# Kernel optimization log

Measured on AMD Instinct MI355X. Metric: run time of the kernel, lower is better.

## Reference

```python
import jax, jax.numpy as jnp
import numpy as np

D = 128      # d_model
H = 8        # n_heads
HD = D // H  # head_dim = 16
E = 256      # n_experts
R = 32       # kv_lora_rank
B, T = 4, 512
EPS = 1e-6


def _dense_init(k, fi, fo):
    s = float(1.0 / np.sqrt(fi))
    return jax.random.uniform(k, (fi, fo), minval=-s, maxval=s, dtype=jnp.float32)


def setup_inputs() -> dict:
    key = jax.random.key(0)
    ks = jax.random.split(key, 16)
    rng = np.random.RandomState(42)
    Q, _ = np.linalg.qr(rng.randn(D, D))
    glim = float(np.sqrt(6.0 / (D + D)))
    return {
        'x': jax.random.normal(ks[0], (B, T, D), dtype=jnp.float32),
        'g1': jnp.ones((D,), jnp.float32),
        'qW': _dense_init(ks[1], D, D), 'qb': jnp.zeros((D,), jnp.float32),
        'kdW': _dense_init(ks[2], D, R), 'kdb': jnp.zeros((R,), jnp.float32),
        'kuW': _dense_init(ks[3], R, 2 * D), 'kub': jnp.zeros((2 * D,), jnp.float32),
        'oW': _dense_init(ks[4], D, D), 'ob': jnp.zeros((D,), jnp.float32),
        'rot': jnp.asarray(Q, jnp.float32),
        'tq_scale': jnp.ones((D,), jnp.float32),
        's1W': _dense_init(ks[5], D, D), 's1b': jnp.zeros((D,), jnp.float32),
        's2W': _dense_init(ks[6], D, D), 's2b': jnp.zeros((D,), jnp.float32),
        'g2': jnp.ones((D,), jnp.float32),
        'gateW': _dense_init(ks[7], D, E), 'gateb': jnp.zeros((E,), jnp.float32),
        'expW': jax.random.uniform(ks[8], (E, D, D), minval=-glim, maxval=glim, dtype=jnp.float32),
        'm1W': _dense_init(ks[9], D, D), 'm1b': jnp.zeros((D,), jnp.float32),
        'm2W': _dense_init(ks[10], D, D), 'm2b': jnp.zeros((D,), jnp.float32),
    }


def _rmsnorm(x, g):
    return g * (x / jnp.sqrt(jnp.mean(x * x, axis=-1, keepdims=True) + EPS))


def _swiglu(x, w1, b1, w2, b2):
    gate = x @ w1 + b1
    return gate * jax.nn.sigmoid(gate) * (x @ w2 + b2)


def _mla(x, qW, qb, kdW, kdb, kuW, kub, oW, ob):
    b, t = x.shape[0], x.shape[1]
    q = (x @ qW + qb).reshape(b, t, H, HD)
    kv = ((x @ kdW + kdb) @ kuW + kub).reshape(b, t, H, 2 * HD)
    k, v = jnp.split(kv, 2, axis=-1)
    q = jax.nn.elu(q) + 1.0
    k = jax.nn.elu(k) + 1.0
    # linear attention: context[b,h,d,e] = sum_t k[b,t,h,d] v[b,t,h,e]
    context = jnp.einsum('bthd,bthe->bhde', k, v)
    out = jnp.einsum('bthd,bhde->bthe', q, context)
    k_sum = jnp.sum(k, axis=1)  # [b,h,d]
    z = 1.0 / (jnp.einsum('bthd,bhd->bth', q, k_sum) + EPS)
    out = out * z[..., None]
    return out.reshape(b, t, D) @ oW + ob


def _turbo_quant(x, rot, scale):
    x = x @ rot
    mag = jnp.sqrt(jnp.mean(x * x, axis=-1, keepdims=True) + EPS)
    phase = x / mag
    qp = jnp.clip(phase * 127.0, -127.0, 127.0) / 127.0
    phase = jax.lax.stop_gradient(qp - phase) + phase  # straight-through
    return phase * mag * scale


def _moe(h, gateW, gateb, expW, m1W, m1b, m2W, m2b):
    gate_scores = jax.nn.softmax(h @ gateW + gateb, axis=-1)  # [B,T,E]
    top_vals, top_idx = jax.lax.top_k(gate_scores, 2)
    top_w = top_vals / (jnp.sum(top_vals, axis=-1, keepdims=True) + EPS)
    # dense all-expert compute as in the original module
    eo = jnp.einsum('btd,edo->bteo', h, expW)  # [B,T,E,D]
    mask = jnp.sum(jax.nn.one_hot(top_idx, E, dtype=h.dtype) * top_w[..., None], axis=2)  # [B,T,E]
    wavg = jnp.einsum('bteo,bte->bto', eo, mask)
    wavg = _swiglu(wavg, m1W, m1b, m2W, m2b)
    diff_sq = jnp.square(eo - wavg[:, :, None, :])
    wvar = jnp.einsum('bteo,bte->bto', diff_sq, mask)
    consensus = jnp.exp(-jnp.mean(wvar, axis=-1))  # [B,T]
    return wavg, consensus


def reference(x, g1, qW, qb, kdW, kdb, kuW, kub, oW, ob, rot, tq_scale,
              s1W, s1b, s2W, s2b, g2, gateW, gateb, expW, m1W, m1b, m2W, m2b):
    attn_out = _turbo_quant(_mla(_rmsnorm(x, g1), qW, qb, kdW, kdb, kuW, kub, oW, ob), rot, tq_scale)
    x = x + _swiglu(attn_out, s1W, s1b, s2W, s2b)
    moe_out, consensus = _moe(_rmsnorm(x, g2), gateW, gateb, expW, m1W, m1b, m2W, m2b)
    return x + moe_out, consensus
```

## Files before the change

### kernel.cpp

```cpp
#include <hip/hip_runtime.h>
#include <hip/hip_bf16.h>
#include <math.h>

static constexpr int Dd   = 128;
static constexpr int NH   = 8;
static constexpr int HD   = 16;
static constexpr int NE   = 256;
static constexpr int RR   = 32;
static constexpr int BB   = 4;
static constexpr int TT   = 512;
static constexpr int NTOK = BB * TT;
static constexpr int TPB  = 4;
static constexpr int SLOTS = 256;
#define EPSF 1e-6f

__device__ __forceinline__ float elu1(float v) { return v > 0.f ? v + 1.f : expf(v); }
__device__ __forceinline__ float sigm(float v) { return 1.f / (1.f + expf(-v)); }

__global__ __launch_bounds__(256) void k_init(
    const float* __restrict__ oW, const float* __restrict__ ob,
    const float* __restrict__ rot,
    const float* __restrict__ kdW, const float* __restrict__ kdb,
    const float* __restrict__ kuW, const float* __restrict__ kub,
    float* __restrict__ oR, float* __restrict__ bR,
    float* __restrict__ kvW, float* __restrict__ bkv,
    float* __restrict__ ctx, float* __restrict__ ksum, int* __restrict__ cnt) {
  const int blk = blockIdx.x, tid = threadIdx.x;
  if (blk < 64) {
    int row = blk * 2 + (tid >> 7), col = tid & 127;
    const float* ow = oW + row * 128;
    float acc = 0.f;
#pragma unroll 8
    for (int k = 0; k < 128; k++) acc += ow[k] * rot[k * 128 + col];
    oR[row * 128 + col] = acc;
  } else if (blk == 64) {
    if (tid < 128) {
      float acc = 0.f;
#pragma unroll 8
      for (int k = 0; k < 128; k++) acc += ob[k] * rot[k * 128 + tid];
      bR[tid] = acc;
    }
    {
      float acc = kub[tid];
#pragma unroll
      for (int k = 0; k < 32; k++) acc += kdb[k] * kuW[k * 256 + tid];
      bkv[tid] = acc;
    }
    for (int i = tid; i < 32 * 256; i += 256) ctx[i] = 0.f;
    for (int i = tid; i < 512; i += 256) ksum[i] = 0.f;
    cnt[tid] = 0;
  } else {
    int idx = (blk - 65) * 256 + tid;
    int row = idx >> 8, col = idx & 255;
    const float* kw = kdW + row * 32;
    float acc = 0.f;
#pragma unroll
    for (int k = 0; k < 32; k++) acc += kw[k] * kuW[k * 256 + col];
    kvW[row * 256 + col] = acc;
  }
}

__global__ __launch_bounds__(768) void k_pre(
    const float* __restrict__ x, const float* __restrict__ g1,
    const float* __restrict__ qW, const float* __restrict__ qb,
    const float* __restrict__ kvW, const float* __restrict__ bkv,
    float* __restrict__ qbuf, float* __restrict__ kvbuf) {
  const int tid = threadIdx.x;
  const int lane = tid & 63;
  const int n0 = blockIdx.x * TPB;

  __shared__ float4 xgT[128];
  __shared__ float4 qpart[128];
  __shared__ float4 kvpart[256];
  __shared__ float4 rtmp[2];

  if (tid < 128) {
    int j = tid;
    float g1j = g1[j];
    float v[4], xg[4];
#pragma unroll
    for (int t = 0; t < 4; t++) {
      float xv = x[(n0 + t) * Dd + j];
      v[t] = xv * xv;
      xg[t] = xv * g1j;
    }
    xgT[j] = make_float4(xg[0], xg[1], xg[2], xg[3]);
#pragma unroll
    for (int o = 32; o > 0; o >>= 1) {
#pragma unroll
      for (int t = 0; t < 4; t++) v[t] += __shfl_xor(v[t], o, 64);
    }
    if (lane == 0) rtmp[tid >> 6] = make_float4(v[0], v[1], v[2], v[3]);
  }
  __syncthreads();

  float a0 = 0, a1 = 0, a2 = 0, a3 = 0;
  const bool isq = tid < 256;
  int j, kh;
  if (isq) {
    j = tid & 127; kh = tid >> 7;
    const float* Wp = qW + (kh * 64) * Dd + j;
    const float4* hb = xgT + kh * 64;
#pragma unroll 16
    for (int i = 0; i < 64; i++) {
      float4 h4 = hb[i];
      float w = Wp[i * Dd];
      a0 += h4.x * w; a1 += h4.y * w; a2 += h4.z * w; a3 += h4.w * w;
    }
    if (kh) qpart[j] = make_float4(a0, a1, a2, a3);
  } else {
    int u = tid - 256;
    j = u & 255; kh = u >> 8;
    const float* Wp = kvW + (kh * 64) * 256 + j;
    const float4* hb = xgT + kh * 64;
#pragma unroll 16
    for (int i = 0; i < 64; i++) {
      float4 h4 = hb[i];
      float w = Wp[i * 256];
      a0 += h4.x * w; a1 += h4.y * w; a2 += h4.z * w; a3 += h4.w * w;
    }
    if (kh) kvpart[j] = make_float4(a0, a1, a2, a3);
  }
  __syncthreads();

  if (kh == 0) {
    float r[4];
#pragma unroll
    for (int t = 0; t < 4; t++) {
      float ss = ((const float*)&rtmp[0])[t] + ((const float*)&rtmp[1])[t];
      r[t] = rsqrtf(ss * (1.f / 128.f) + EPSF);
    }
    if (isq) {
      float4 p = qpart[j];
      float bb = qb[j];
      qbuf[(n0 + 0) * Dd + j] = elu1((a0 + p.x) * r[0] + bb);
      qbuf[(n0 + 1) * Dd + j] = elu1((a1 + p.y) * r[1] + bb);
      qbuf[(n0 + 2) * Dd + j] = elu1((a2 + p.z) * r[2] + bb);
      qbuf[(n0 + 3) * Dd + j] = elu1((a3 + p.w) * r[3] + bb);
    } else {
      float4 p = kvpart[j];
      float bb = bkv[j];
      bool isk = (j & 31) < 16;
      float v0 = (a0 + p.x) * r[0] + bb, v1 = (a1 + p.y) * r[1] + bb;
      float v2 = (a2 + p.z) * r[2] + bb, v3 = (a3 + p.w) * r[3] + bb;
      kvbuf[(n0 + 0) * 256 + j] = isk ? elu1(v0) : v0;
      kvbuf[(n0 + 1) * 256 + j] = isk ? elu1(v1) : v1;
      kvbuf[(n0 + 2) * 256 + j] = isk ? elu1(v2) : v2;
      kvbuf[(n0 + 3) * 256 + j] = isk ? elu1(v3) : v3;
    }
  }
}

__global__ __launch_bounds__(256) void k_ctx(const float* __restrict__ kv,
                                             float* __restrict__ ctx,
                                             float* __restrict__ ksum) {
  const int blk = blockIdx.x;
  const int bh = blk >> 3, c = blk & 7;
  const int b = bh >> 3, h = bh & 7;
  const int tid = threadIdx.x;
  const int d = tid >> 4, e = tid & 15;
  __shared__ float sh[64 * 32];
#pragma unroll
  for (int r = 0; r < 8; r++) {
    int lin = r * 256 + tid;
    int tok = lin >> 5, off = lin & 31;
    sh[lin] = kv[((b * TT + c * 64 + tok) * 256) + h * 32 + off];
  }
  __syncthreads();
  float acc = 0.f, ks = 0.f;
#pragma unroll 4
  for (int t = 0; t < 64; t++) {
    float kk = sh[t * 32 + d];
    acc += kk * sh[t * 32 + 16 + e];
    ks += kk;
  }
  atomicAdd(&ctx[bh * 256 + d * 16 + e], acc);
  if (e == 0) atomicAdd(&ksum[bh * 16 + d], ks);
}

__global__ __launch_bounds__(512) void k_mid(
    const float* __restrict__ x, const float* __restrict__ qbuf,
    const float* __restrict__ ctx, const float* __restrict__ ksum,
    const float* __restrict__ oR, const float* __restrict__ bR,
    const float* __restrict__ tqs,
    const float* __restrict__ s1W, const float* __restrict__ s1b,
    const float* __restrict__ s2W, const float* __restrict__ s2b,
    const float* __restrict__ g2, const float* __restrict__ gateW,
    const float* __restrict__ gateb,
    float* __restrict__ xnbuf, float* __restrict__ h2buf,
    float* __restrict__ gw, int* __restrict__ tokslot,
    int* __restrict__ slottok, int* __restrict__ cnt) {
  const int tid = threadIdx.x;
  const int j = tid & 127, g = tid >> 7;
  const int lane = tid & 63;
  const int n0 = blockIdx.x * TPB;
  const int b = n0 >> 9;

  __shared__ float4 bufA[128], bufB[128];
  __shared__ float4 part[3][128];
  __shared__ float4 gpart[256];
  __shared__ float4 rtmp[2];
  __shared__ float wvS[4][4]; __shared__ int wiS[4][4];
  __shared__ float zS[4][4];

  float xres[4];
  if (tid < 128) {
#pragma unroll
    for (int t = 0; t < 4; t++) xres[t] = x[(n0 + t) * Dd + j];
  }

  ((float*)&bufA[j])[g] = qbuf[(n0 + g) * Dd + j];
  __syncthreads();

  if (tid < 128) {
    int h = j >> 4, e = j & 15;
    const float* cpt = ctx + (b * NH + h) * 256;
    const float* kpt = ksum + (b * NH + h) * 16;
    float num[4] = {0, 0, 0, 0}, den[4] = {0, 0, 0, 0};
#pragma unroll
    for (int d = 0; d < 16; d++) {
      float cx = cpt[d * 16 + e], ks = kpt[d];
      float4 q4 = bufA[h * 16 + d];
      num[0] += q4.x * cx; num[1] += q4.y * cx; num[2] += q4.z * cx; num[3] += q4.w * cx;
      den[0] += q4.x * ks; den[1] += q4.y * ks; den[2] += q4.z * ks; den[3] += q4.w * ks;
    }
#pragma unroll
    for (int t = 0; t < 4; t++) ((float*)&bufB[j])[t] = num[t] / (den[t] + EPSF);
  }
  __syncthreads();

  {
    float a0 = 0, a1 = 0, a2 = 0, a3 = 0;
    const float* Wp = oR + (g * 32) * Dd + j;
#pragma unroll 16
    for (int i = 0; i < 32; i++) {
      float4 h4 = bufB[g * 32 + i];
      float w = Wp[i * Dd];
      a0 += h4.x * w; a1 += h4.y * w; a2 += h4.z * w; a3 += h4.w * w;
    }
    if (g) part[g - 1][j] = make_float4(a0, a1, a2, a3);
    __syncthreads();
    float tot[4];
    if (g == 0) {
      float4 p0 = part[0][j], p1 = part[1][j], p2 = part[2][j];
      float bb = bR[j];
      tot[0] = a0 + p0.x + p1.x + p2.x + bb; tot[1] = a1 + p0.y + p1.y + p2.y + bb;
      tot[2] = a2 + p0.z + p1.z + p2.z + bb; tot[3] = a3 + p0.w + p1.w + p2.w + bb;
      float v[4];
#pragma unroll
      for (int t = 0; t < 4; t++) v[t] = tot[t] * tot[t];
#pragma unroll
      for (int o = 32; o > 0; o >>= 1) {
#pragma unroll
        for (int t = 0; t < 4; t++) v[t] += __shfl_xor(v[t], o, 64);
      }
      if (lane == 0) rtmp[tid >> 6] = make_float4(v[0], v[1], v[2], v[3]);
    }
    __syncthreads();
    if (g == 0) {
      float scj = tqs[j];
#pragma unroll
      for (int t = 0; t < 4; t++) {
        float ss = ((const float*)&rtmp[0])[t] + ((const float*)&rtmp[1])[t];
        float mag = sqrtf(ss * (1.f / 128.f) + EPSF);
        float zc = fminf(fmaxf(tot[t], -mag), mag);
        ((float*)&bufA[j])[t] = zc * scj;
      }
    }
    __syncthreads();
  }

  {
    float a0 = 0, a1 = 0, a2 = 0, a3 = 0;
    const float* Wp = (g < 2 ? s1W : s2W) + ((g & 1) * 64) * Dd + j;
#pragma unroll 16
    for (int i = 0; i < 64; i++) {
      float4 h4 = bufA[(g & 1) * 64 + i];
      float w = Wp[i * Dd];
      a0 += h4.x * w; a1 += h4.y * w; a2 += h4.z * w; a3 += h4.w * w;
    }
    if (g) part[g - 1][j] = make_float4(a0, a1, a2, a3);
    __syncthreads();
    if (g == 0) {
      float b1 = s1b[j], b2 = s2b[j];
      float4 p0 = part[0][j], p1 = part[1][j], p2 = part[2][j];
      float gv[4], uv[4], xn[4], v[4];
      gv[0] = a0 + p0.x + b1; gv[1] = a1 + p0.y + b1;
      gv[2] = a2 + p0.z + b1; gv[3] = a3 + p0.w + b1;
      uv[0] = p1.x + p2.x + b2; uv[1] = p1.y + p2.y + b2;
      uv[2] = p1.z + p2.z + b2; uv[3] = p1.w + p2.w + b2;
      float g2j = g2[j];
#pragma unroll
      for (int t = 0; t < 4; t++) {
        xn[t] = xres[t] + gv[t] * sigm(gv[t]) * uv[t];
        xnbuf[(n0 + t) * Dd + j] = xn[t];
        ((float*)&bufB[j])[t] = g2j * xn[t];
        v[t] = xn[t] * xn[t];
      }
#pragma unroll
      for (int o = 32; o > 0; o >>= 1) {
#pragma unroll
        for (int t = 0; t < 4; t++) v[t] += __shfl_xor(v[t], o, 64);
      }
      if (lane == 0) rtmp[tid >> 6] = make_float4(v[0], v[1], v[2], v[3]);
    }
    __syncthreads();
  }

  float val[4];
  float r2[4];
  {
    int col = tid & 255, kh = tid >> 8;
    float a0 = 0, a1 = 0, a2 = 0, a3 = 0;
    const float* Wp = gateW + (kh * 64) * NE + col;
#pragma unroll 16
    for (int i = 0; i < 64; i++) {
      float4 h4 = bufB[kh * 64 + i];
      float w = Wp[i * NE];
      a0 += h4.x * w; a1 += h4.y * w; a2 += h4.z * w; a3 += h4.w * w;
    }
    if (kh) gpart[col] = make_float4(a0, a1, a2, a3);
    __syncthreads();
#pragma unroll
    for (int t = 0; t < 4; t++) {
      float ss = ((const float*)&rtmp[0])[t] + ((const float*)&rtmp[1])[t];
      r2[t] = rsqrtf(ss * (1.f / 128.f) + EPSF);
    }
    if (!kh) {
      float4 p = gpart[col];
      float bb = gateb[col];
      val[0] = (a0 + p.x) * r2[0] + bb; val[1] = (a1 + p.y) * r2[1] + bb;
      val[2] = (a2 + p.z) * r2[2] + bb; val[3] = (a3 + p.w) * r2[3] + bb;
    }
    if (tid < 128) {
#pragma unroll
      for (int t = 0; t < 4; t++)
        h2buf[(n0 + t) * Dd + j] = ((const float*)&bufB[j])[t] * r2[t];
    }
  }
  __syncthreads();

  float m1[4]; int i1[4];
  {
    if (tid < 256) {
      float bv[4]; int bi[4];
#pragma unroll
      for (int t = 0; t < 4; t++) { bv[t] = val[t]; bi[t] = tid; }
#pragma unroll
      for (int o = 32; o > 0; o >>= 1) {
#pragma unroll
        for (int t = 0; t < 4; t++) {
          float wv = __shfl_xor(bv[t], o, 64);
          int wi = __shfl_xor(bi[t], o, 64);
          if (wv > bv[t] || (wv == bv[t] && wi < bi[t])) { bv[t] = wv; bi[t] = wi; }
        }
      }
      if (lane == 0) {
#pragma unroll
        for (int t = 0; t < 4; t++) { wvS[tid >> 6][t] = bv[t]; wiS[tid >> 6][t] = bi[t]; }
      }
    }
    __syncthreads();
    if (tid < 256) {
#pragma unroll
      for (int t = 0; t < 4; t++) {
        m1[t] = wvS[0][t]; i1[t] = wiS[0][t];
#pragma unroll
        for (int w = 1; w < 4; w++) {
          float cv = wvS[w][t]; int ci = wiS[w][t];
          if (cv > m1[t] || (cv == m1[t] && ci < i1[t])) { m1[t] = cv; i1[t] = ci; }
        }
      }
    }
    __syncthreads();
  }
  float m2[4]; int i2[4];
  {
    if (tid < 256) {
      float bv[4]; int bi[4];
#pragma unroll
      for (int t = 0; t < 4; t++) {
        bv[t] = (tid == i1[t]) ? -INFINITY : val[t];
        bi[t] = tid;
      }
#pragma unroll
      for (int o = 32; o > 0; o >>= 1) {
#pragma unroll
        for (int t = 0; t < 4; t++) {
          float wv = __shfl_xor(bv[t], o, 64);
          int wi = __shfl_xor(bi[t], o, 64);
          if (wv > bv[t] || (wv == bv[t] && wi < bi[t])) { bv[t] = wv; bi[t] = wi; }
        }
      }
      if (lane == 0) {
#pragma unroll
        for (int t = 0; t < 4; t++) { wvS[tid >> 6][t] = bv[t]; wiS[tid >> 6][t] = bi[t]; }
      }
    }
    __syncthreads();
    if (tid < 256) {
#pragma unroll
      for (int t = 0; t < 4; t++) {
        m2[t] = wvS[0][t]; i2[t] = wiS[0][t];
#pragma unroll
        for (int w = 1; w < 4; w++) {
          float cv = wvS[w][t]; int ci = wiS[w][t];
          if (cv > m2[t] || (cv == m2[t] && ci < i2[t])) { m2[t] = cv; i2[t] = ci; }
        }
      }
    }
    __syncthreads();
  }
  {
    if (tid < 256) {
      float v[4];
#pragma unroll
      for (int t = 0; t < 4; t++) v[t] = expf(val[t] - m1[t]);
#pragma unroll
      for (int o = 32; o > 0; o >>= 1) {
#pragma unroll
        for (int t = 0; t < 4; t++) v[t] += __shfl_xor(v[t], o, 64);
      }
      if (lane == 0) {
#pragma unroll
        for (int t = 0; t < 4; t++) zS[tid >> 6][t] = v[t];
      }
    }
    __syncthreads();
  }
  if (tid < 4) {
    int t = tid, tok = n0 + t;
    float Z = zS[0][t] + zS[1][t] + zS[2][t] + zS[3][t];
    float p1 = 1.f / Z;
    float p2 = expf(m2[t] - m1[t]) / Z;
    float s = p1 + p2 + EPSF;
    int e1 = i1[t], e2 = i2[t];
    int s1 = atomicAdd(&cnt[e1], 1); if (s1 > SLOTS - 1) s1 = SLOTS - 1;
    int s2 = atomicAdd(&cnt[e2], 1); if (s2 > SLOTS - 1) s2 = SLOTS - 1;
    int sl1 = e1 * SLOTS + s1, sl2 = e2 * SLOTS + s2;
    slottok[sl1] = tok; slottok[sl2] = tok;
    tokslot[tok * 2] = sl1; tokslot[tok * 2 + 1] = sl2;
    gw[tok * 2] = p1 / s; gw[tok * 2 + 1] = p2 / s;
  }
}

__global__ __launch_bounds__(512) void k_exp(const float* __restrict__ h2buf,
                                             const int* __restrict__ slottok,
                                             const int* __restrict__ cnt,
                                             const float* __restrict__ expW,
                                             float* __restrict__ ybuf) {
  const int e = blockIdx.x;
  int n = cnt[e]; if (n > SLOTS) n = SLOTS;
  if (n == 0) return;
  const int base = e * SLOTS;
  const int tid = threadIdx.x;
  const int j = tid & 127, g = tid >> 7;
  __shared__ __align__(16) float hT[128 * 20];
  const float* Wp = expW + (size_t)e * Dd * Dd + j;
  for (int t0 = 0; t0 < n; t0 += 16) {
    int m = n - t0; if (m > 16) m = 16;
    __syncthreads();
    for (int tt = g; tt < m; tt += 4) {
      int tok = slottok[base + t0 + tt];
      hT[j * 20 + tt] = h2buf[tok * Dd + j];
    }
    __syncthreads();
    float acc[4] = {0, 0, 0, 0};
#pragma unroll 8
    for (int i = 0; i < 128; i++) {
      float w = Wp[i * Dd];
      float4 h4 = *(const float4*)&hT[i * 20 + g * 4];
      acc[0] += h4.x * w; acc[1] += h4.y * w; acc[2] += h4.z * w; acc[3] += h4.w * w;
    }
#pragma unroll
    for (int k = 0; k < 4; k++) {
      int tt = g * 4 + k;
      if (tt < m) ybuf[(size_t)(base + t0 + tt) * Dd + j] = acc[k];
    }
  }
}

__global__ __launch_bounds__(512) void k_post(
    const float* __restrict__ xnbuf, const float* __restrict__ ybuf,
    const int* __restrict__ tokslot, const float* __restrict__ gw,
    const float* __restrict__ m1W, const float* __restrict__ m1b,
    const float* __restrict__ m2W, const float* __restrict__ m2b,
    float* __restrict__ out) {
  const int tid = threadIdx.x;
  const int j = tid & 127, g = tid >> 7;
  const int lane = tid & 63;
  const int n0 = blockIdx.x * TPB;

  __shared__ float4 y1T[128], y2T[128], inT[128], sT[128];
  __shared__ float4 part[3][128];
  __shared__ float4 rtmp[2];
  __shared__ int sSlot[4][2];
  __shared__ float sWt[4][2];

  if (tid < 4) {
    sSlot[tid][0] = tokslot[(n0 + tid) * 2];
    sSlot[tid][1] = tokslot[(n0 + tid) * 2 + 1];
    sWt[tid][0] = gw[(n0 + tid) * 2];
    sWt[tid][1] = gw[(n0 + tid) * 2 + 1];
  }
  __syncthreads();

  {
    float y1 = ybuf[(size_t)sSlot[g][0] * Dd + j];
    float y2 = ybuf[(size_t)sSlot[g][1] * Dd + j];
    ((float*)&y1T[j])[g] = y1;
    ((float*)&y2T[j])[g] = y2;
    ((float*)&inT[j])[g] = sWt[g][0] * y1 + sWt[g][1] * y2;
  }
  __syncthreads();

  {
    float a0 = 0, a1 = 0, a2 = 0, a3 = 0;
    const float* Wp = (g < 2 ? m1W : m2W) + ((g & 1) * 64) * Dd + j;
#pragma unroll 16
    for (int i = 0; i < 64; i++) {
      float4 h4 = inT[(g & 1) * 64 + i];
      float w = Wp[i * Dd];
      a0 += h4.x * w; a1 += h4.y * w; a2 += h4.z * w; a3 += h4.w * w;
    }
    if (g) part[g - 1][j] = make_float4(a0, a1, a2, a3);
    __syncthreads();
    if (g == 0) {
      float b1 = m1b[j], b2 = m2b[j];
      float4 p0 = part[0][j], p1 = part[1][j], p2 = part[2][j];
      float gv[4], uv[4];
      gv[0] = a0 + p0.x + b1; gv[1] = a1 + p0.y + b1;
      gv[2] = a2 + p0.z + b1; gv[3] = a3 + p0.w + b1;
      uv[0] = p1.x + p2.x + b2; uv[1] = p1.y + p2.y + b2;
      uv[2] = p1.z + p2.z + b2; uv[3] = p1.w + p2.w + b2;
#pragma unroll
      for (int t = 0; t < 4; t++) {
        float sv = gv[t] * sigm(gv[t]) * uv[t];
        ((float*)&sT[j])[t] = sv;
        out[(n0 + t) * Dd + j] = xnbuf[(n0 + t) * Dd + j] + sv;
      }
    }
    __syncthreads();
  }

  if (tid < 128) {
    float v[4];
#pragma unroll
    for (int t = 0; t < 4; t++) {
      float sv = ((const float*)&sT[j])[t];
      float d1 = ((const float*)&y1T[j])[t] - sv;
      float d2 = ((const float*)&y2T[j])[t] - sv;
      v[t] = sWt[t][0] * d1 * d1 + sWt[t][1] * d2 * d2;
    }
#pragma unroll
    for (int o = 32; o > 0; o >>= 1) {
#pragma unroll
      for (int t = 0; t < 4; t++) v[t] += __shfl_xor(v[t], o, 64);
    }
    if (lane == 0) rtmp[tid >> 6] = make_float4(v[0], v[1], v[2], v[3]);
  }
  __syncthreads();
  if (tid < 4) {
    float s = ((const float*)&rtmp[0])[tid] + ((const float*)&rtmp[1])[tid];
    out[NTOK * Dd + n0 + tid] = expf(-s * (1.f / 128.f));
  }
}

extern "C" void kernel_launch(void* const* d_in, const int* in_sizes, int n_in,
                              void* d_out, int out_size, void* d_ws, size_t ws_size,
                              hipStream_t stream) {
  const float* x   = (const float*)d_in[0];
  const float* g1  = (const float*)d_in[1];
  const float* qW  = (const float*)d_in[2];
  const float* qb  = (const float*)d_in[3];
  const float* kdW = (const float*)d_in[4];
  const float* kdb = (const float*)d_in[5];
  const float* kuW = (const float*)d_in[6];
  const float* kub = (const float*)d_in[7];
  const float* oW  = (const float*)d_in[8];
  const float* ob  = (const float*)d_in[9];
  const float* rot = (const float*)d_in[10];
  const float* tqs = (const float*)d_in[11];
  const float* s1W = (const float*)d_in[12];
  const float* s1b = (const float*)d_in[13];
  const float* s2W = (const float*)d_in[14];
  const float* s2b = (const float*)d_in[15];
  const float* g2  = (const float*)d_in[16];
  const float* gW  = (const float*)d_in[17];
  const float* gb  = (const float*)d_in[18];
  const float* eW  = (const float*)d_in[19];
  const float* m1W = (const float*)d_in[20];
  const float* m1b = (const float*)d_in[21];
  const float* m2W = (const float*)d_in[22];
  const float* m2b = (const float*)d_in[23];
  float* out = (float*)d_out;
  float* ws  = (float*)d_ws;

  float* qbuf   = ws;
  float* kvbuf  = ws + 262144;
  float* ctx    = ws + 786432;
  float* ksum   = ws + 794624;
  float* h2buf  = ws + 795136;
  float* xnbuf  = ws + 1057280;
  float* gw     = ws + 1319424;
  float* oRb    = ws + 1323520;
  float* bRb    = ws + 1339904;
  float* kvW    = ws + 1340032;
  float* bkv    = ws + 1372800;
  int*   cnt     = (int*)(ws + 1373056);
  int*   tokslot = (int*)(ws + 1373312);
  int*   slottok = (int*)(ws + 1377408);
  float* ybuf   = ws + 1442944;

  k_init<<<193, 256, 0, stream>>>(oW, ob, rot, kdW, kdb, kuW, kub,
                                  oRb, bRb, kvW, bkv, ctx, ksum, cnt);
  k_pre<<<NTOK / TPB, 768, 0, stream>>>(x, g1, qW, qb, kvW, bkv, qbuf, kvbuf);
  k_ctx<<<256, 256, 0, stream>>>(kvbuf, ctx, ksum);
  k_mid<<<NTOK / TPB, 512, 0, stream>>>(x, qbuf, ctx, ksum, oRb, bRb, tqs,
                                        s1W, s1b, s2W, s2b, g2, gW, gb,
                                        xnbuf, h2buf, gw, tokslot, slottok, cnt);
  k_exp<<<NE, 512, 0, stream>>>(h2buf, slottok, cnt, eW, ybuf);
  k_post<<<NTOK / TPB, 512, 0, stream>>>(xnbuf, ybuf, tokslot, gw,
                                         m1W, m1b, m2W, m2b, out);
}
```

Baseline: 168.5 us.

## Eliminate init kernel by fusing low-rank KV projection and weight prep into neighbors

```diff
diff --git a/kernel.cpp b/kernel.cpp
--- a/kernel.cpp
+++ b/kernel.cpp
@@ -4,12 +4,10 @@
 
 static constexpr int Dd   = 128;
 static constexpr int NH   = 8;
-static constexpr int HD   = 16;
 static constexpr int NE   = 256;
 static constexpr int RR   = 32;
-static constexpr int BB   = 4;
 static constexpr int TT   = 512;
-static constexpr int NTOK = BB * TT;
+static constexpr int NTOK = 2048;
 static constexpr int TPB  = 4;
 static constexpr int SLOTS = 256;
 #define EPSF 1e-6f
@@ -17,165 +15,173 @@
 __device__ __forceinline__ float elu1(float v) { return v > 0.f ? v + 1.f : expf(v); }
 __device__ __forceinline__ float sigm(float v) { return 1.f / (1.f + expf(-v)); }
 
-__global__ __launch_bounds__(256) void k_init(
-    const float* __restrict__ oW, const float* __restrict__ ob,
-    const float* __restrict__ rot,
+__global__ __launch_bounds__(512) void k_pre(
+    const float* __restrict__ x, const float* __restrict__ g1,
+    const float* __restrict__ qW, const float* __restrict__ qb,
     const float* __restrict__ kdW, const float* __restrict__ kdb,
     const float* __restrict__ kuW, const float* __restrict__ kub,
-    float* __restrict__ oR, float* __restrict__ bR,
-    float* __restrict__ kvW, float* __restrict__ bkv,
+    float* __restrict__ qbuf, float* __restrict__ kvbuf,
     float* __restrict__ ctx, float* __restrict__ ksum, int* __restrict__ cnt) {
-  const int blk = blockIdx.x, tid = threadIdx.x;
-  if (blk < 64) {
-    int row = blk * 2 + (tid >> 7), col = tid & 127;
+  const int tid = threadIdx.x;
+  const int j = tid & 127, g = tid >> 7;
+  const int lane = tid & 63;
+  const int n0 = blockIdx.x * TPB;
+
+  __shared__ float4 h1T[128];
+  __shared__ float4 part[3][128];
+  __shared__ float4 kpart[8][32];
+  __shared__ float4 kdT[32];
+  __shared__ float4 kupart[256];
+  __shared__ float4 rtmp[2];
+
+  if (blockIdx.x == 0) {
+    for (int i = tid; i < 32 * 256; i += 512) ctx[i] = 0.f;
+    ksum[tid] = 0.f;
+    if (tid < 256) cnt[tid] = 0;
+  }
+
+  float xv[4];
+  if (tid < 128) {
+    float v[4];
+#pragma unroll
+    for (int t = 0; t < 4; t++) { xv[t] = x[(n0 + t) * Dd + j]; v[t] = xv[t] * xv[t]; }
+#pragma unroll
+    for (int o = 32; o > 0; o >>= 1) {
+#pragma unroll
+      for (int t = 0; t < 4; t++) v[t] += __shfl_xor(v[t], o, 64);
+    }
+    if (lane == 0) rtmp[tid >> 6] = make_float4(v[0], v[1], v[2], v[3]);
+  }
+  __syncthreads();
+  if (tid < 128) {
+    float g1j = g1[j];
+#pragma unroll
+    for (int t = 0; t < 4; t++) {
+      float ss = ((const float*)&rtmp[0])[t] + ((const float*)&rtmp[1])[t];
+      ((float*)&h1T[j])[t] = g1j * xv[t] * rsqrtf(ss * (1.f / 128.f) + EPSF);
+    }
+  }
+  __syncthreads();
+
+  {
+    float a0 = 0, a1 = 0, a2 = 0, a3 = 0;
+    const float* Wp = qW + (g * 32) * Dd + j;
+#pragma unroll 16
+    for (int i = 0; i < 32; i++) {
+      float4 h4 = h1T[g * 32 + i];
+      float w = Wp[i * Dd];
+      a0 += h4.x * w; a1 += h4.y * w; a2 += h4.z * w; a3 += h4.w * w;
+    }
+    if (g) part[g - 1][j] = make_float4(a0, a1, a2, a3);
+    __syncthreads();
+    if (g == 0) {
+      float4 p0 = part[0][j], p1 = part[1][j], p2 = part[2][j];
+      float bb = qb[j];
+      qbuf[(n0 + 0) * Dd + j] = elu1(a0 + p0.x + p1.x + p2.x + bb);
+      qbuf[(n0 + 1) * Dd + j] = elu1(a1 + p0.y + p1.y + p2.y + bb);
+      qbuf[(n0 + 2) * Dd + j] = elu1(a2 + p0.z + p1.z + p2.z + bb);
+      qbuf[(n0 + 3) * Dd + j] = elu1(a3 + p0.w + p1.w + p2.w + bb);
+    }
+    __syncthreads();
+  }
+
+  if (tid < 256) {
+    int col = tid & 31, ksp = tid >> 5;
+    float a0 = 0, a1 = 0, a2 = 0, a3 = 0;
+    const float* Wp = kdW + (ksp * 16) * RR + col;
+#pragma unroll
+    for (int i = 0; i < 16; i++) {
+      float4 h4 = h1T[ksp * 16 + i];
+      float w = Wp[i * RR];
+      a0 += h4.x * w; a1 += h4.y * w; a2 += h4.z * w; a3 += h4.w * w;
+    }
+    kpart[ksp][col] = make_float4(a0, a1, a2, a3);
+  }
+  __syncthreads();
+  if (tid < 32) {
+    float bb = kdb[tid];
+    float s0 = bb, s1 = bb, s2 = bb, s3 = bb;
+#pragma unroll
+    for (int k = 0; k < 8; k++) {
+      float4 p = kpart[k][tid];
+      s0 += p.x; s1 += p.y; s2 += p.z; s3 += p.w;
+    }
+    kdT[tid] = make_float4(s0, s1, s2, s3);
+  }
+  __syncthreads();
+
+  {
+    int col = tid & 255, kh = tid >> 8;
+    float a0 = 0, a1 = 0, a2 = 0, a3 = 0;
+    const float* Wp = kuW + (kh * 16) * 256 + col;
+#pragma unroll
+    for (int r = 0; r < 16; r++) {
+      float4 k4 = kdT[kh * 16 + r];
+      float w = Wp[r * 256];
+      a0 += k4.x * w; a1 += k4.y * w; a2 += k4.z * w; a3 += k4.w * w;
+    }
+    if (kh) kupart[col] = make_float4(a0, a1, a2, a3);
+    __syncthreads();
+    if (!kh) {
+      float4 p = kupart[col];
+      float bb = kub[col];
+      bool isk = (col & 31) < 16;
+      float v0 = a0 + p.x + bb, v1 = a1 + p.y + bb, v2 = a2 + p.z + bb, v3 = a3 + p.w + bb;
+      kvbuf[(n0 + 0) * 256 + col] = isk ? elu1(v0) : v0;
+      kvbuf[(n0 + 1) * 256 + col] = isk ? elu1(v1) : v1;
+      kvbuf[(n0 + 2) * 256 + col] = isk ? elu1(v2) : v2;
+      kvbuf[(n0 + 3) * 256 + col] = isk ? elu1(v3) : v3;
+    }
+  }
+}
+
+__global__ __launch_bounds__(256) void k_ctx(const float* __restrict__ kv,
+                                             float* __restrict__ ctx,
+                                             float* __restrict__ ksum,
+                                             const float* __restrict__ oW,
+                                             const float* __restrict__ ob,
+                                             const float* __restrict__ rot,
+                                             float* __restrict__ oR,
+                                             float* __restrict__ bR) {
+  const int blk = blockIdx.x;
+  const int tid = threadIdx.x;
+  if (blk < 256) {
+    const int bh = blk >> 3, c = blk & 7;
+    const int b = bh >> 3, h = bh & 7;
+    const int d = tid >> 4, e = tid & 15;
+    __shared__ float sh[64 * 32];
+#pragma unroll
+    for (int r = 0; r < 8; r++) {
+      int lin = r * 256 + tid;
+      int tok = lin >> 5, off = lin & 31;
+      sh[lin] = kv[((b * TT + c * 64 + tok) * 256) + h * 32 + off];
+    }
+    __syncthreads();
+    float acc = 0.f, ks = 0.f;
+#pragma unroll 4
+    for (int t = 0; t < 64; t++) {
+      float kk = sh[t * 32 + d];
+      acc += kk * sh[t * 32 + 16 + e];
+      ks += kk;
+    }
+    atomicAdd(&ctx[bh * 256 + d * 16 + e], acc);
+    if (e == 0) atomicAdd(&ksum[bh * 16 + d], ks);
+  } else if (blk < 320) {
+    int idx = (blk - 256) * 256 + tid;
+    int row = idx >> 7, col = idx & 127;
     const float* ow = oW + row * 128;
     float acc = 0.f;
 #pragma unroll 8
     for (int k = 0; k < 128; k++) acc += ow[k] * rot[k * 128 + col];
     oR[row * 128 + col] = acc;
-  } else if (blk == 64) {
+  } else {
     if (tid < 128) {
       float acc = 0.f;
 #pragma unroll 8
       for (int k = 0; k < 128; k++) acc += ob[k] * rot[k * 128 + tid];
       bR[tid] = acc;
     }
-    {
-      float acc = kub[tid];
-#pragma unroll
-      for (int k = 0; k < 32; k++) acc += kdb[k] * kuW[k * 256 + tid];
-      bkv[tid] = acc;
-    }
-    for (int i = tid; i < 32 * 256; i += 256) ctx[i] = 0.f;
-    for (int i = tid; i < 512; i += 256) ksum[i] = 0.f;
-    cnt[tid] = 0;
-  } else {
-    int idx = (blk - 65) * 256 + tid;
-    int row = idx >> 8, col = idx & 255;
-    const float* kw = kdW + row * 32;
-    float acc = 0.f;
-#pragma unroll
-    for (int k = 0; k < 32; k++) acc += kw[k] * kuW[k * 256 + col];
-    kvW[row * 256 + col] = acc;
-  }
-}
-
-__global__ __launch_bounds__(768) void k_pre(
-    const float* __restrict__ x, const float* __restrict__ g1,
-    const float* __restrict__ qW, const float* __restrict__ qb,
-    const float* __restrict__ kvW, const float* __restrict__ bkv,
-    float* __restrict__ qbuf, float* __restrict__ kvbuf) {
-  const int tid = threadIdx.x;
-  const int lane = tid & 63;
-  const int n0 = blockIdx.x * TPB;
-
-  __shared__ float4 xgT[128];
-  __shared__ float4 qpart[128];
-  __shared__ float4 kvpart[256];
-  __shared__ float4 rtmp[2];
-
-  if (tid < 128) {
-    int j = tid;
-    float g1j = g1[j];
-    float v[4], xg[4];
-#pragma unroll
-    for (int t = 0; t < 4; t++) {
-      float xv = x[(n0 + t) * Dd + j];
-      v[t] = xv * xv;
-      xg[t] = xv * g1j;
-    }
-    xgT[j] = make_float4(xg[0], xg[1], xg[2], xg[3]);
-#pragma unroll
-    for (int o = 32; o > 0; o >>= 1) {
-#pragma unroll
-      for (int t = 0; t < 4; t++) v[t] += __shfl_xor(v[t], o, 64);
-    }
-    if (lane == 0) rtmp[tid >> 6] = make_float4(v[0], v[1], v[2], v[3]);
-  }
-  __syncthreads();
-
-  float a0 = 0, a1 = 0, a2 = 0, a3 = 0;
-  const bool isq = tid < 256;
-  int j, kh;
-  if (isq) {
-    j = tid & 127; kh = tid >> 7;
-    const float* Wp = qW + (kh * 64) * Dd + j;
-    const float4* hb = xgT + kh * 64;
-#pragma unroll 16
-    for (int i = 0; i < 64; i++) {
-      float4 h4 = hb[i];
-      float w = Wp[i * Dd];
-      a0 += h4.x * w; a1 += h4.y * w; a2 += h4.z * w; a3 += h4.w * w;
-    }
-    if (kh) qpart[j] = make_float4(a0, a1, a2, a3);
-  } else {
-    int u = tid - 256;
-    j = u & 255; kh = u >> 8;
-    const float* Wp = kvW + (kh * 64) * 256 + j;
-    const float4* hb = xgT + kh * 64;
-#pragma unroll 16
-    for (int i = 0; i < 64; i++) {
-      float4 h4 = hb[i];
-      float w = Wp[i * 256];
-      a0 += h4.x * w; a1 += h4.y * w; a2 += h4.z * w; a3 += h4.w * w;
-    }
-    if (kh) kvpart[j] = make_float4(a0, a1, a2, a3);
-  }
-  __syncthreads();
-
-  if (kh == 0) {
-    float r[4];
-#pragma unroll
-    for (int t = 0; t < 4; t++) {
-      float ss = ((const float*)&rtmp[0])[t] + ((const float*)&rtmp[1])[t];
-      r[t] = rsqrtf(ss * (1.f / 128.f) + EPSF);
-    }
-    if (isq) {
-      float4 p = qpart[j];
-      float bb = qb[j];
-      qbuf[(n0 + 0) * Dd + j] = elu1((a0 + p.x) * r[0] + bb);
-      qbuf[(n0 + 1) * Dd + j] = elu1((a1 + p.y) * r[1] + bb);
-      qbuf[(n0 + 2) * Dd + j] = elu1((a2 + p.z) * r[2] + bb);
-      qbuf[(n0 + 3) * Dd + j] = elu1((a3 + p.w) * r[3] + bb);
-    } else {
-      float4 p = kvpart[j];
-      float bb = bkv[j];
-      bool isk = (j & 31) < 16;
-      float v0 = (a0 + p.x) * r[0] + bb, v1 = (a1 + p.y) * r[1] + bb;
-      float v2 = (a2 + p.z) * r[2] + bb, v3 = (a3 + p.w) * r[3] + bb;
-      kvbuf[(n0 + 0) * 256 + j] = isk ? elu1(v0) : v0;
-      kvbuf[(n0 + 1) * 256 + j] = isk ? elu1(v1) : v1;
-      kvbuf[(n0 + 2) * 256 + j] = isk ? elu1(v2) : v2;
-      kvbuf[(n0 + 3) * 256 + j] = isk ? elu1(v3) : v3;
-    }
-  }
-}
-
-__global__ __launch_bounds__(256) void k_ctx(const float* __restrict__ kv,
-                                             float* __restrict__ ctx,
-                                             float* __restrict__ ksum) {
-  const int blk = blockIdx.x;
-  const int bh = blk >> 3, c = blk & 7;
-  const int b = bh >> 3, h = bh & 7;
-  const int tid = threadIdx.x;
-  const int d = tid >> 4, e = tid & 15;
-  __shared__ float sh[64 * 32];
-#pragma unroll
-  for (int r = 0; r < 8; r++) {
-    int lin = r * 256 + tid;
-    int tok = lin >> 5, off = lin & 31;
-    sh[lin] = kv[((b * TT + c * 64 + tok) * 256) + h * 32 + off];
-  }
-  __syncthreads();
-  float acc = 0.f, ks = 0.f;
-#pragma unroll 4
-  for (int t = 0; t < 64; t++) {
-    float kk = sh[t * 32 + d];
-    acc += kk * sh[t * 32 + 16 + e];
-    ks += kk;
-  }
-  atomicAdd(&ctx[bh * 256 + d * 16 + e], acc);
-  if (e == 0) atomicAdd(&ksum[bh * 16 + d], ks);
+  }
 }
 
 __global__ __launch_bounds__(512) void k_mid(
@@ -605,17 +611,14 @@
   float* gw     = ws + 1319424;
   float* oRb    = ws + 1323520;
   float* bRb    = ws + 1339904;
-  float* kvW    = ws + 1340032;
-  float* bkv    = ws + 1372800;
   int*   cnt     = (int*)(ws + 1373056);
   int*   tokslot = (int*)(ws + 1373312);
   int*   slottok = (int*)(ws + 1377408);
   float* ybuf   = ws + 1442944;
 
-  k_init<<<193, 256, 0, stream>>>(oW, ob, rot, kdW, kdb, kuW, kub,
-                                  oRb, bRb, kvW, bkv, ctx, ksum, cnt);
-  k_pre<<<NTOK / TPB, 768, 0, stream>>>(x, g1, qW, qb, kvW, bkv, qbuf, kvbuf);
-  k_ctx<<<256, 256, 0, stream>>>(kvbuf, ctx, ksum);
+  k_pre<<<NTOK / TPB, 512, 0, stream>>>(x, g1, qW, qb, kdW, kdb, kuW, kub,
+                                        qbuf, kvbuf, ctx, ksum, cnt);
+  k_ctx<<<321, 256, 0, stream>>>(kvbuf, ctx, ksum, oW, ob, rot, oRb, bRb);
   k_mid<<<NTOK / TPB, 512, 0, stream>>>(x, qbuf, ctx, ksum, oRb, bRb, tqs,
                                         s1W, s1b, s2W, s2b, g2, gW, gb,
                                         xnbuf, h2buf, gw, tokslot, slottok, cnt);
```

Measured after the change: 167.2 us. No clear change (-0.7%).
